# Kernel tuning notes

Hardware: AMD Instinct MI355X
Metric: run time of the kernel (lower is better)

## Reference

```python
import jax, jax.numpy as jnp
import numpy as np

OUT = 50000   # out_features = connectivity rows
IN = 50000    # in_features  = connectivity cols
NNZ = 1_600_000  # avg degree 32
B = 512       # batch (leading dims of x)


def setup_inputs() -> dict:
    key = jax.random.key(0)
    k1, k2, k3, k4 = jax.random.split(key, 4)
    x = jax.random.normal(k1, (B, IN), dtype=jnp.float32)
    rows = jax.random.randint(k2, (NNZ,), 0, OUT, dtype=jnp.int32)
    cols = jax.random.randint(k3, (NNZ,), 0, IN, dtype=jnp.int32)
    indices = jnp.stack([rows, cols])            # [2, NNZ] COO indices
    values = jax.random.normal(k4, (NNZ,), dtype=jnp.float32)
    bias = jnp.zeros((OUT, 1), dtype=jnp.float32)  # module initializes bias to zeros
    return {"x": x, "indices": indices, "values": values, "bias": bias}


def reference(x, indices, values, bias):
    # feature_dim=-1: permute features to dim 0 -> x_t is (IN, B)
    row, col = indices[0], indices[1]
    x_t = x.T                                    # (IN, B)
    # spmm: for each nnz, values[e] * x_t[col[e]] accumulated into row[e]
    contrib = values[:, None] * x_t[col]         # (NNZ, B)
    y = jax.ops.segment_sum(contrib, row, num_segments=OUT)  # (OUT, B)
    y = y + bias                                 # bias is (OUT, 1), broadcasts
    return y.T                                   # permute back -> (B, OUT)
```

## Files before the change

### kernel.cpp

```cpp
#include <hip/hip_runtime.h>
#include <hip/hip_bf16.h>


typedef float  f32x4 __attribute__((ext_vector_type(4)));
typedef unsigned int u32x4 __attribute__((ext_vector_type(4)));

__global__ __launch_bounds__(256) void transpose_bf16_v2(
        const float* __restrict__ in,
        __hip_bfloat16* __restrict__ out,
        int rows, int cols) {
    __shared__ __hip_bfloat16 T[64][72];
    const int t  = threadIdx.x;
    const int c0 = blockIdx.x * 64;
    const int r0 = blockIdx.y * 64;

    {
        const int tx = t & 15, ty = t >> 4;
        const int c = c0 + tx * 4;
        for (int p = 0; p < 4; ++p) {
            const int rl = ty + p * 16;
            const int r = r0 + rl;
            float fx = 0.f, fy = 0.f, fz = 0.f, fw = 0.f;
            if (r < rows && c + 3 < cols) {
                f32x4 f = __builtin_nontemporal_load(
                    (const f32x4*)(in + (size_t)r * cols + c));
                fx = f.x; fy = f.y; fz = f.z; fw = f.w;
            } else if (r < rows) {
                const float* p0 = in + (size_t)r * cols;
                if (c + 0 < cols) fx = p0[c + 0];
                if (c + 1 < cols) fy = p0[c + 1];
                if (c + 2 < cols) fz = p0[c + 2];
                if (c + 3 < cols) fw = p0[c + 3];
            }
            T[tx * 4 + 0][rl] = __float2bfloat16(fx);
            T[tx * 4 + 1][rl] = __float2bfloat16(fy);
            T[tx * 4 + 2][rl] = __float2bfloat16(fz);
            T[tx * 4 + 3][rl] = __float2bfloat16(fw);
        }
    }
    __syncthreads();
    {
        const int cl0 = t >> 3;
        const int rq  = t & 7;
        const int rl  = rq * 8;
        const int r   = r0 + rl;
        for (int q = 0; q < 2; ++q) {
            const int cl = q * 32 + cl0;
            const int c  = c0 + cl;
            if (c < cols) {
                if (r + 7 < rows) {
                    *(uint4*)(out + (size_t)c * rows + r) =
                        *(const uint4*)&T[cl][rl];
                } else {
                    for (int j = 0; j < 8 && r + j < rows; ++j)
                        out[(size_t)c * rows + r + j] = T[cl][rl + j];
                }
            }
        }
    }
}

__global__ __launch_bounds__(256) void transpose32_v2(
        const float* __restrict__ in,
        float* __restrict__ out,
        int rows, int cols) {
    __shared__ float T[64][68];
    const int t  = threadIdx.x;
    const int c0 = blockIdx.x * 64;
    const int r0 = blockIdx.y * 64;

    {
        const int tx = t & 15, ty = t >> 4;
        const int c = c0 + tx * 4;
        for (int p = 0; p < 4; ++p) {
            const int rl = ty + p * 16;
            const int r = r0 + rl;
            float fx = 0.f, fy = 0.f, fz = 0.f, fw = 0.f;
            if (r < rows && c + 3 < cols) {
                f32x4 f = __builtin_nontemporal_load(
                    (const f32x4*)(in + (size_t)r * cols + c));
                fx = f.x; fy = f.y; fz = f.z; fw = f.w;
            } else if (r < rows) {
                const float* p0 = in + (size_t)r * cols;
                if (c + 0 < cols) fx = p0[c + 0];
                if (c + 1 < cols) fy = p0[c + 1];
                if (c + 2 < cols) fz = p0[c + 2];
                if (c + 3 < cols) fw = p0[c + 3];
            }
            T[tx * 4 + 0][rl] = fx;
            T[tx * 4 + 1][rl] = fy;
            T[tx * 4 + 2][rl] = fz;
            T[tx * 4 + 3][rl] = fw;
        }
    }
    __syncthreads();
    {
        const int rq  = t & 15;
        const int cl0 = t >> 4;
        const int rl  = rq * 4;
        const int r   = r0 + rl;
        for (int p = 0; p < 4; ++p) {
            const int cl = p * 16 + cl0;
            const int c  = c0 + cl;
            if (c < cols) {
                if (r + 3 < rows) {
                    f32x4 f;
                    f.x = T[cl][rl + 0]; f.y = T[cl][rl + 1];
                    f.z = T[cl][rl + 2]; f.w = T[cl][rl + 3];
                    __builtin_nontemporal_store(
                        f, (f32x4*)(out + (size_t)c * rows + r));
                } else {
                    for (int j = 0; j < 4 && r + j < rows; ++j)
                        out[(size_t)c * rows + r + j] = T[cl][rl + j];
                }
            }
        }
    }
}

__global__ void zero_i32_kernel(int* __restrict__ p, int n) {
    int i = blockIdx.x * blockDim.x + threadIdx.x;
    if (i < n) p[i] = 0;
}

__global__ void hist_kernel(const int* __restrict__ rows, int nnz,
                            int* __restrict__ counts) {
    int e = blockIdx.x * blockDim.x + threadIdx.x;
    if (e < nnz) {
        int r = __builtin_nontemporal_load(rows + e);
        atomicAdd(&counts[r], 1);
    }
}

#define SCAN_T 256
#define SCAN_CHUNK 2048

__global__ __launch_bounds__(SCAN_T) void scan1_kernel(
        const int* __restrict__ counts, int* __restrict__ offsets,
        int* __restrict__ bsum, int n) {
    __shared__ int sdata[SCAN_T];
    int t = threadIdx.x;
    int base_i = blockIdx.x * SCAN_CHUNK + t * 8;
    int vals[8];
    int tot = 0;
#pragma unroll
    for (int j = 0; j < 8; ++j) {
        int i = base_i + j;
        int v = (i < n) ? counts[i] : 0;
        tot += v;
        vals[j] = tot;
    }
    sdata[t] = tot;
    __syncthreads();
    for (int off = 1; off < SCAN_T; off <<= 1) {
        int x = (t >= off) ? sdata[t - off] : 0;
        __syncthreads();
        sdata[t] += x;
        __syncthreads();
    }
    int tbase = (t > 0) ? sdata[t - 1] : 0;
#pragma unroll
    for (int j = 0; j < 8; ++j) {
        int i = base_i + j;
        if (i < n) offsets[i + 1] = tbase + vals[j];
    }
    if (t == SCAN_T - 1) bsum[blockIdx.x] = sdata[SCAN_T - 1];
}

__global__ void scan2_kernel(int* __restrict__ bsum, int nb) {
    if (threadIdx.x == 0 && blockIdx.x == 0) {
        int run = 0;
        for (int i = 0; i < nb; ++i) { int v = bsum[i]; bsum[i] = run; run += v; }
    }
}

__global__ void scan3_kernel(int* __restrict__ offsets,
                             const int* __restrict__ bsum, int n) {
    int i = blockIdx.x * blockDim.x + threadIdx.x;
    if (i == 0) offsets[0] = 0;
    if (i < n) offsets[i + 1] += bsum[i / SCAN_CHUNK];
}

__global__ void scatter_kernel(const int* __restrict__ rows,
                               const int* __restrict__ cols,
                               const float* __restrict__ vals, int nnz,
                               const int* __restrict__ offsets,
                               int* __restrict__ counts,
                               int2* __restrict__ edges) {
    int e = blockIdx.x * blockDim.x + threadIdx.x;
    if (e < nnz) {
        int r = __builtin_nontemporal_load(rows + e);
        int c = __builtin_nontemporal_load(cols + e);
        float v = __builtin_nontemporal_load(vals + e);
        int p = offsets[r] + atomicSub(&counts[r], 1) - 1;
        edges[p] = make_int2(c, __float_as_int(v));
    }
}

__device__ __forceinline__ float bf_lo(unsigned u) {
    return __uint_as_float(u << 16);
}
__device__ __forceinline__ float bf_hi(unsigned u) {
    return __uint_as_float(u & 0xffff0000u);
}

__global__ __launch_bounds__(256) void spmm_kernel(
        const ushort* __restrict__ xT,
        const int* __restrict__ offsets,
        const int2* __restrict__ edges,
        const float* __restrict__ bias,
        float* __restrict__ y,
        int B, int OUTn) {
    const int lane = threadIdx.x & 63;
    const int r = blockIdx.x * 4 + (threadIdx.x >> 6);
    if (r >= OUTn) return;
    const int e0 = offsets[r];
    const int e1 = offsets[r + 1];
    const float bv = bias[r];
    const ushort* xb = xT + (size_t)(lane << 3);

    float a0 = 0.f, a1 = 0.f, a2 = 0.f, a3 = 0.f;
    float a4 = 0.f, a5 = 0.f, a6 = 0.f, a7 = 0.f;

    int e = e0;
    for (; e + 2 <= e1; e += 2) {
        const long long p0 =
            __builtin_nontemporal_load((const long long*)(edges + e));
        const long long p1 =
            __builtin_nontemporal_load((const long long*)(edges + e + 1));
        const int   c0 = (int)(unsigned)p0;
        const float v0 = __int_as_float((int)(p0 >> 32));
        const int   c1 = (int)(unsigned)p1;
        const float v1 = __int_as_float((int)(p1 >> 32));
        const uint4 u0 = *(const uint4*)(xb + (size_t)c0 * B);
        const uint4 u1 = *(const uint4*)(xb + (size_t)c1 * B);
        a0 += v0 * bf_lo(u0.x); a1 += v0 * bf_hi(u0.x);
        a2 += v0 * bf_lo(u0.y); a3 += v0 * bf_hi(u0.y);
        a4 += v0 * bf_lo(u0.z); a5 += v0 * bf_hi(u0.z);
        a6 += v0 * bf_lo(u0.w); a7 += v0 * bf_hi(u0.w);
        a0 += v1 * bf_lo(u1.x); a1 += v1 * bf_hi(u1.x);
        a2 += v1 * bf_lo(u1.y); a3 += v1 * bf_hi(u1.y);
        a4 += v1 * bf_lo(u1.z); a5 += v1 * bf_hi(u1.z);
        a6 += v1 * bf_lo(u1.w); a7 += v1 * bf_hi(u1.w);
    }
    if (e < e1) {
        const long long p0 =
            __builtin_nontemporal_load((const long long*)(edges + e));
        const int   c0 = (int)(unsigned)p0;
        const float v0 = __int_as_float((int)(p0 >> 32));
        const uint4 u0 = *(const uint4*)(xb + (size_t)c0 * B);
        a0 += v0 * bf_lo(u0.x); a1 += v0 * bf_hi(u0.x);
        a2 += v0 * bf_lo(u0.y); a3 += v0 * bf_hi(u0.y);
        a4 += v0 * bf_lo(u0.z); a5 += v0 * bf_hi(u0.z);
        a6 += v0 * bf_lo(u0.w); a7 += v0 * bf_hi(u0.w);
    }

    float* yp = y + (size_t)r * B + (size_t)(lane << 3);
    f32x4 o0, o1;
    o0.x = a0 + bv; o0.y = a1 + bv; o0.z = a2 + bv; o0.w = a3 + bv;
    o1.x = a4 + bv; o1.y = a5 + bv; o1.z = a6 + bv; o1.w = a7 + bv;
    __builtin_nontemporal_store(o0, (f32x4*)(yp));
    __builtin_nontemporal_store(o1, (f32x4*)(yp + 4));
}

extern "C" void kernel_launch(void* const* d_in, const int* in_sizes, int n_in,
                              void* d_out, int out_size, void* d_ws, size_t ws_size,
                              hipStream_t stream) {
    const float* x       = (const float*)d_in[0];
    const int*   indices = (const int*)  d_in[1];
    const float* values  = (const float*)d_in[2];
    const float* bias    = (const float*)d_in[3];

    float* out = (float*)d_out;

    const int NNZ = in_sizes[2];
    const int OUT = in_sizes[3];
    const int B   = out_size / OUT;
    const int IN  = (int)((size_t)in_sizes[0] / (size_t)B);

    const int* rows = indices;
    const int* cols = indices + NNZ;

    char* ws = (char*)d_ws;
    __hip_bfloat16* xT = (__hip_bfloat16*)ws;  ws += (size_t)IN * B * sizeof(__hip_bfloat16);
    float* y       = (float*)ws;  ws += (size_t)OUT * B * sizeof(float);
    int2*  edges   = (int2*)ws;   ws += (size_t)NNZ * sizeof(int2);
    int*   counts  = (int*)ws;    ws += (size_t)OUT * sizeof(int);
    int*   offsets = (int*)ws;    ws += (size_t)(OUT + 1) * sizeof(int);
    int*   bsum    = (int*)ws;    ws += 256 * sizeof(int);

    const int nchunks = (OUT + SCAN_CHUNK - 1) / SCAN_CHUNK;

    transpose_bf16_v2<<<dim3((IN + 63) / 64, (B + 63) / 64), 256, 0, stream>>>(
        x, xT, B, IN);

    zero_i32_kernel<<<(OUT + 255) / 256, 256, 0, stream>>>(counts, OUT);
    hist_kernel<<<(NNZ + 255) / 256, 256, 0, stream>>>(rows, NNZ, counts);
    scan1_kernel<<<nchunks, SCAN_T, 0, stream>>>(counts, offsets, bsum, OUT);
    scan2_kernel<<<1, 64, 0, stream>>>(bsum, nchunks);
    scan3_kernel<<<(OUT + 255) / 256, 256, 0, stream>>>(offsets, bsum, OUT);
    scatter_kernel<<<(NNZ + 255) / 256, 256, 0, stream>>>(
        rows, cols, values, NNZ, offsets, counts, edges);

    spmm_kernel<<<(OUT + 3) / 4, 256, 0, stream>>>(
        (const ushort*)xT, offsets, edges, bias, y, B, OUT);

    transpose32_v2<<<dim3((B + 63) / 64, (OUT + 63) / 64), 256, 0, stream>>>(
        y, out, OUT, B);
}
```

Measured before the change: 627.3 us.

## Bucket CSR edges by column tile within each row for gather locality

The histogram and scatter now key each edge by (row, column tile of 2048 columns), so edges within a row come out grouped by column range. The offsets array grows to OUT*NT entries and the scans run over it. The aim is to make gathers of xT rows more localized in cache across concurrent wavefronts. The change also drops several nontemporal load and store hints in the final transpose and the spmm kernel. The cost is a much larger count/offset array (about 25x) and longer scan, zero and atomic passes.

```diff
diff --git a/kernel.cpp b/kernel.cpp
--- a/kernel.cpp
+++ b/kernel.cpp
@@ -2,8 +2,9 @@
 #include <hip/hip_bf16.h>
 
 
-typedef float  f32x4 __attribute__((ext_vector_type(4)));
-typedef unsigned int u32x4 __attribute__((ext_vector_type(4)));
+typedef float f32x4 __attribute__((ext_vector_type(4)));
+
+#define CT_SHIFT 11
 
 __global__ __launch_bounds__(256) void transpose_bf16_v2(
         const float* __restrict__ in,
@@ -77,8 +78,7 @@
             const int r = r0 + rl;
             float fx = 0.f, fy = 0.f, fz = 0.f, fw = 0.f;
             if (r < rows && c + 3 < cols) {
-                f32x4 f = __builtin_nontemporal_load(
-                    (const f32x4*)(in + (size_t)r * cols + c));
+                const float4 f = *(const float4*)(in + (size_t)r * cols + c);
                 fx = f.x; fy = f.y; fz = f.z; fw = f.w;
             } else if (r < rows) {
                 const float* p0 = in + (size_t)r * cols;
@@ -123,17 +123,20 @@
     if (i < n) p[i] = 0;
 }
 
-__global__ void hist_kernel(const int* __restrict__ rows, int nnz,
-                            int* __restrict__ counts) {
+__global__ void hist_kernel(const int* __restrict__ rows,
+                            const int* __restrict__ cols, int nnz,
+                            int* __restrict__ counts, int NT) {
     int e = blockIdx.x * blockDim.x + threadIdx.x;
     if (e < nnz) {
         int r = __builtin_nontemporal_load(rows + e);
-        atomicAdd(&counts[r], 1);
+        int c = __builtin_nontemporal_load(cols + e);
+        atomicAdd(&counts[r * NT + (c >> CT_SHIFT)], 1);
     }
 }
 
 #define SCAN_T 256
 #define SCAN_CHUNK 2048
+#define MAX_CHUNKS 1024
 
 __global__ __launch_bounds__(SCAN_T) void scan1_kernel(
         const int* __restrict__ counts, int* __restrict__ offsets,
@@ -186,13 +189,14 @@
                                const float* __restrict__ vals, int nnz,
                                const int* __restrict__ offsets,
                                int* __restrict__ counts,
-                               int2* __restrict__ edges) {
+                               int2* __restrict__ edges, int NT) {
     int e = blockIdx.x * blockDim.x + threadIdx.x;
     if (e < nnz) {
         int r = __builtin_nontemporal_load(rows + e);
         int c = __builtin_nontemporal_load(cols + e);
         float v = __builtin_nontemporal_load(vals + e);
-        int p = offsets[r] + atomicSub(&counts[r], 1) - 1;
+        int k = r * NT + (c >> CT_SHIFT);
+        int p = offsets[k] + atomicSub(&counts[k], 1) - 1;
         edges[p] = make_int2(c, __float_as_int(v));
     }
 }
@@ -210,12 +214,12 @@
         const int2* __restrict__ edges,
         const float* __restrict__ bias,
         float* __restrict__ y,
-        int B, int OUTn) {
+        int B, int OUTn, int NT) {
     const int lane = threadIdx.x & 63;
     const int r = blockIdx.x * 4 + (threadIdx.x >> 6);
     if (r >= OUTn) return;
-    const int e0 = offsets[r];
-    const int e1 = offsets[r + 1];
+    const int e0 = offsets[(size_t)r * NT];
+    const int e1 = offsets[(size_t)(r + 1) * NT];
     const float bv = bias[r];
     const ushort* xb = xT + (size_t)(lane << 3);
 
@@ -224,16 +228,12 @@
 
     int e = e0;
     for (; e + 2 <= e1; e += 2) {
-        const long long p0 =
-            __builtin_nontemporal_load((const long long*)(edges + e));
-        const long long p1 =
-            __builtin_nontemporal_load((const long long*)(edges + e + 1));
-        const int   c0 = (int)(unsigned)p0;
-        const float v0 = __int_as_float((int)(p0 >> 32));
-        const int   c1 = (int)(unsigned)p1;
-        const float v1 = __int_as_float((int)(p1 >> 32));
-        const uint4 u0 = *(const uint4*)(xb + (size_t)c0 * B);
-        const uint4 u1 = *(const uint4*)(xb + (size_t)c1 * B);
+        const int2 d0 = edges[e];
+        const int2 d1 = edges[e + 1];
+        const uint4 u0 = *(const uint4*)(xb + (size_t)d0.x * B);
+        const uint4 u1 = *(const uint4*)(xb + (size_t)d1.x * B);
+        const float v0 = __int_as_float(d0.y);
+        const float v1 = __int_as_float(d1.y);
         a0 += v0 * bf_lo(u0.x); a1 += v0 * bf_hi(u0.x);
         a2 += v0 * bf_lo(u0.y); a3 += v0 * bf_hi(u0.y);
         a4 += v0 * bf_lo(u0.z); a5 += v0 * bf_hi(u0.z);
@@ -244,11 +244,9 @@
         a6 += v1 * bf_lo(u1.w); a7 += v1 * bf_hi(u1.w);
     }
     if (e < e1) {
-        const long long p0 =
-            __builtin_nontemporal_load((const long long*)(edges + e));
-        const int   c0 = (int)(unsigned)p0;
-        const float v0 = __int_as_float((int)(p0 >> 32));
-        const uint4 u0 = *(const uint4*)(xb + (size_t)c0 * B);
+        const int2 d0 = edges[e];
+        const uint4 u0 = *(const uint4*)(xb + (size_t)d0.x * B);
+        const float v0 = __int_as_float(d0.y);
         a0 += v0 * bf_lo(u0.x); a1 += v0 * bf_hi(u0.x);
         a2 += v0 * bf_lo(u0.y); a3 += v0 * bf_hi(u0.y);
         a4 += v0 * bf_lo(u0.z); a5 += v0 * bf_hi(u0.z);
@@ -256,11 +254,8 @@
     }
 
     float* yp = y + (size_t)r * B + (size_t)(lane << 3);
-    f32x4 o0, o1;
-    o0.x = a0 + bv; o0.y = a1 + bv; o0.z = a2 + bv; o0.w = a3 + bv;
-    o1.x = a4 + bv; o1.y = a5 + bv; o1.z = a6 + bv; o1.w = a7 + bv;
-    __builtin_nontemporal_store(o0, (f32x4*)(yp));
-    __builtin_nontemporal_store(o1, (f32x4*)(yp + 4));
+    *(float4*)(yp)     = make_float4(a0 + bv, a1 + bv, a2 + bv, a3 + bv);
+    *(float4*)(yp + 4) = make_float4(a4 + bv, a5 + bv, a6 + bv, a7 + bv);
 }
 
 extern "C" void kernel_launch(void* const* d_in, const int* in_sizes, int n_in,
@@ -281,29 +276,32 @@
     const int* rows = indices;
     const int* cols = indices + NNZ;
 
+    const int NT   = (IN + (1 << CT_SHIFT) - 1) >> CT_SHIFT;
+    const int NKEY = OUT * NT;
+
     char* ws = (char*)d_ws;
     __hip_bfloat16* xT = (__hip_bfloat16*)ws;  ws += (size_t)IN * B * sizeof(__hip_bfloat16);
     float* y       = (float*)ws;  ws += (size_t)OUT * B * sizeof(float);
     int2*  edges   = (int2*)ws;   ws += (size_t)NNZ * sizeof(int2);
-    int*   counts  = (int*)ws;    ws += (size_t)OUT * sizeof(int);
-    int*   offsets = (int*)ws;    ws += (size_t)(OUT + 1) * sizeof(int);
-    int*   bsum    = (int*)ws;    ws += 256 * sizeof(int);
-
-    const int nchunks = (OUT + SCAN_CHUNK - 1) / SCAN_CHUNK;
+    int*   counts  = (int*)ws;    ws += (size_t)NKEY * sizeof(int);
+    int*   offsets = (int*)ws;    ws += ((size_t)NKEY + 4) * sizeof(int);
+    int*   bsum    = (int*)ws;    ws += MAX_CHUNKS * sizeof(int);
+
+    const int nchunks = (NKEY + SCAN_CHUNK - 1) / SCAN_CHUNK;
 
     transpose_bf16_v2<<<dim3((IN + 63) / 64, (B + 63) / 64), 256, 0, stream>>>(
         x, xT, B, IN);
 
-    zero_i32_kernel<<<(OUT + 255) / 256, 256, 0, stream>>>(counts, OUT);
-    hist_kernel<<<(NNZ + 255) / 256, 256, 0, stream>>>(rows, NNZ, counts);
-    scan1_kernel<<<nchunks, SCAN_T, 0, stream>>>(counts, offsets, bsum, OUT);
+    zero_i32_kernel<<<(NKEY + 255) / 256, 256, 0, stream>>>(counts, NKEY);
+    hist_kernel<<<(NNZ + 255) / 256, 256, 0, stream>>>(rows, cols, NNZ, counts, NT);
+    scan1_kernel<<<nchunks, SCAN_T, 0, stream>>>(counts, offsets, bsum, NKEY);
     scan2_kernel<<<1, 64, 0, stream>>>(bsum, nchunks);
-    scan3_kernel<<<(OUT + 255) / 256, 256, 0, stream>>>(offsets, bsum, OUT);
+    scan3_kernel<<<(NKEY + 255) / 256, 256, 0, stream>>>(offsets, bsum, NKEY);
     scatter_kernel<<<(NNZ + 255) / 256, 256, 0, stream>>>(
-        rows, cols, values, NNZ, offsets, counts, edges);
+        rows, cols, values, NNZ, offsets, counts, edges, NT);
 
     spmm_kernel<<<(OUT + 3) / 4, 256, 0, stream>>>(
-        (const ushort*)xT, offsets, edges, bias, y, B, OUT);
+        (const ushort*)xT, offsets, edges, bias, y, B, OUT, NT);
 
     transpose32_v2<<<dim3((B + 63) / 64, (OUT + 63) / 64), 256, 0, stream>>>(
         y, out, OUT, B);
```

Result: slower. 649.7 us (+3.6%).
